# Optimization experiments

Measured on AMD Instinct MI355X. Metric: run time of the kernel, lower is better.

The kernel has to match this reference:

```python
import jax, jax.numpy as jnp
import numpy as np

DECAY = 0.99
EPS = 1e-5
COMMIT_W = 1.0


def setup_inputs() -> dict:
    key = jax.random.key(0)
    k1, k2, k3 = jax.random.split(key, 3)
    N, D, K = 65536, 64, 2048
    x = jax.random.normal(k1, (N, D), dtype=jnp.float32)
    embed = jax.random.normal(k2, (K, D), dtype=jnp.float32)
    embed_avg = jax.random.normal(k3, (K, D), dtype=jnp.float32)
    cluster_size = jnp.ones((K,), dtype=jnp.float32)
    return {"x": x, "embed": embed, "embed_avg": embed_avg, "cluster_size": cluster_size}


def reference(x, embed, embed_avg, cluster_size):
    # x: [N, D], embed: [K, D]
    K = embed.shape[0]
    # squared euclidean distances [N, K] (the cdist step)
    x2 = jnp.sum(x * x, axis=-1, keepdims=True)            # [N, 1]
    e2 = jnp.sum(embed * embed, axis=-1)                    # [K]
    dist = x2 - 2.0 * (x @ embed.T) + e2[None, :]           # [N, K]
    embed_ind = jnp.argmin(dist, axis=-1)                   # [N]

    # codebook gather + straight-through estimator
    quantize = embed[embed_ind]                              # [N, D]
    commit_loss = COMMIT_W * jnp.mean((jax.lax.stop_gradient(quantize) - x) ** 2)
    quantize_st = x + jax.lax.stop_gradient(quantize - x)

    # EMA codebook update (scatter / segment-sum, no gradient)
    ones = jnp.ones(embed_ind.shape, dtype=x.dtype)
    counts = jax.ops.segment_sum(ones, embed_ind, num_segments=K)        # [K]
    embed_sum = jax.ops.segment_sum(x, embed_ind, num_segments=K)        # [K, D]
    new_cluster_size = DECAY * cluster_size + (1.0 - DECAY) * counts
    new_embed_avg = DECAY * embed_avg + (1.0 - DECAY) * embed_sum
    n = jnp.sum(new_cluster_size)
    smoothed = (new_cluster_size + EPS) / (n + K * EPS) * n              # laplace smoothing
    new_embed = new_embed_avg / smoothed[:, None]                         # [K, D]

    return quantize_st, commit_loss, embed_ind, new_embed
```

## Files before the change

### kernel.cpp

```cpp
#include <hip/hip_runtime.h>
#include <hip/hip_bf16.h>

#define N_ROWS 65536
#define DIM 64
#define KC 2048
#define NPHH 16
#define DECAY_F 0.99f
#define OMD_F 0.01f
#define EPS_F 1e-5f
#define MARGIN 0.005f

typedef short  s16x8  __attribute__((ext_vector_type(8)));
typedef __bf16 bf16x8 __attribute__((ext_vector_type(8)));
typedef float  f32x4v __attribute__((ext_vector_type(4)));

__device__ __forceinline__ bf16x8 as_bf(s16x8 v) { return __builtin_bit_cast(bf16x8, v); }

static constexpr size_t WS_E2       = 0;
static constexpr size_t WS_SMOOTH   = 2048;
static constexpr size_t WS_OFFS     = 4096;
static constexpr size_t WS_ROWIDS   = 6144;
static constexpr size_t WS_EH       = 71680;
static constexpr size_t WS_EL       = 137216;
static constexpr size_t WS_COUNTS   = 202752;
static constexpr size_t WS_CURS     = 204800;
static constexpr size_t WS_LOSS     = 206848;
static constexpr size_t WS_FLAGCNT  = 206849;
static constexpr size_t WS_ESUM     = 206852;
static constexpr size_t WS_FLAGLIST = 337924;
static constexpr size_t WS_ZERO_CNT = 4098;

__device__ __forceinline__ unsigned short bf16_rne(float f) {
    unsigned u = __float_as_uint(f);
    return (unsigned short)((u + 0x7FFFu + ((u >> 16) & 1u)) >> 16);
}

__global__ __launch_bounds__(256) void vq_prep_e_kernel(
    const float* __restrict__ embed, float* __restrict__ ws) {
    const int tid = threadIdx.x;
    const int lane = tid & 63;
    const int k = blockIdx.x * 4 + (tid >> 6);

    const int gtid = blockIdx.x * 256 + tid;
    if (gtid < (int)WS_ZERO_CNT) ws[WS_COUNTS + gtid] = 0.f;
    ws[WS_ESUM + gtid] = 0.f;

    float v = embed[(size_t)k * DIM + lane];
    float m2v = -2.f * v;
    unsigned short hb = bf16_rne(m2v);
    float hf = __uint_as_float((unsigned)hb << 16);
    unsigned short lb = bf16_rne(m2v - hf);
    ((short*)(ws + WS_EH))[(size_t)k * DIM + lane] = (short)hb;
    ((short*)(ws + WS_EL))[(size_t)k * DIM + lane] = (short)lb;

    float sq = v * v;
#pragma unroll
    for (int off = 32; off > 0; off >>= 1)
        sq += __shfl_down(sq, off, 64);
    if (lane == 0) ws[WS_E2 + k] = sq;
}

__global__ __launch_bounds__(512, 4) void vq_mfma_kernel(
    const float* __restrict__ x,
    const float* __restrict__ embed,
    float* __restrict__ ws,
    float* __restrict__ out_q,
    float* __restrict__ out_ind) {
    __shared__ __attribute__((aligned(16))) short tile_lds[2][2][16][512];
    __shared__ __attribute__((aligned(16))) float e2_lds[KC];
    __shared__ float mb1[128], mb2[128];
    __shared__ int   mi1[128];

    const int tid = threadIdx.x;
    const int lane = tid & 63;
    const int w = tid >> 6;
    const int kh = w >> 2;
    const int wq = w & 3;
    const int row0 = blockIdx.x * 128 + wq * 32;
    const int cr = lane & 15;
    const int g = lane >> 4;

    {
        const float4* s4p = reinterpret_cast<const float4*>(ws + WS_E2);
        *reinterpret_cast<float4*>(&e2_lds[tid * 4]) = s4p[tid];
    }

    s16x8 xh[2][2], xl[2][2];
#pragma unroll
    for (int f = 0; f < 2; ++f) {
#pragma unroll
        for (int kc = 0; kc < 2; ++kc) {
            const float4* p4 = reinterpret_cast<const float4*>(
                x + (size_t)(row0 + f * 16 + cr) * DIM + kc * 32 + g * 8);
            float4 u = p4[0], v = p4[1];
            s16x8 h, l;
            unsigned short hb;
            hb = bf16_rne(u.x); h[0] = (short)hb; l[0] = (short)bf16_rne(u.x - __uint_as_float((unsigned)hb << 16));
            hb = bf16_rne(u.y); h[1] = (short)hb; l[1] = (short)bf16_rne(u.y - __uint_as_float((unsigned)hb << 16));
            hb = bf16_rne(u.z); h[2] = (short)hb; l[2] = (short)bf16_rne(u.z - __uint_as_float((unsigned)hb << 16));
            hb = bf16_rne(u.w); h[3] = (short)hb; l[3] = (short)bf16_rne(u.w - __uint_as_float((unsigned)hb << 16));
            hb = bf16_rne(v.x); h[4] = (short)hb; l[4] = (short)bf16_rne(v.x - __uint_as_float((unsigned)hb << 16));
            hb = bf16_rne(v.y); h[5] = (short)hb; l[5] = (short)bf16_rne(v.y - __uint_as_float((unsigned)hb << 16));
            hb = bf16_rne(v.z); h[6] = (short)hb; l[6] = (short)bf16_rne(v.z - __uint_as_float((unsigned)hb << 16));
            hb = bf16_rne(v.w); h[7] = (short)hb; l[7] = (short)bf16_rne(v.w - __uint_as_float((unsigned)hb << 16));
            xh[f][kc] = h; xl[f][kc] = l;
        }
    }

    const short* ehp = (const short*)(ws + WS_EH);
    const short* elp = (const short*)(ws + WS_EL);

    const short* mat_base = ((wq < 2) ? ehp : elp) + (wq & 1) * 32;

#define STAGE(buf, ph)                                                                  \
    {                                                                                   \
        _Pragma("unroll")                                                               \
        for (int s4 = 0; s4 < 4; ++s4) {                                                \
            const short* gsrc = mat_base +                                              \
                (size_t)(((kh * NPHH + (ph)) * 64) + s4 * 16 + cr) * DIM + g * 8;       \
            __builtin_amdgcn_global_load_lds(                                           \
                (const __attribute__((address_space(1))) void*)gsrc,                    \
                (__attribute__((address_space(3))) void*)(&tile_lds[(buf)][kh][s4 * 4 + wq][0]), \
                16, 0, 0);                                                              \
        }                                                                               \
    }

    STAGE(0, 0);
    __syncthreads();

    float b1[2] = {__builtin_inff(), __builtin_inff()};
    float b2[2] = {__builtin_inff(), __builtin_inff()};
    int   i1[2] = {0, 0};

    f32x4v accA[4][2], accB[4][2];

#define MFMA_PHASE(ph, WACC)                                                            \
    {                                                                                   \
        const int cur_ = (ph) & 1;                                                      \
        if ((ph) + 1 < NPHH) STAGE(cur_ ^ 1, (ph) + 1);                                 \
        __builtin_amdgcn_s_setprio(1);                                                  \
        _Pragma("unroll")                                                               \
        for (int s = 0; s < 4; ++s) {                                                   \
            s16x8 eh0 = *(const s16x8*)(&tile_lds[cur_][kh][s * 4 + 0][lane * 8]);      \
            s16x8 eh1 = *(const s16x8*)(&tile_lds[cur_][kh][s * 4 + 1][lane * 8]);      \
            s16x8 el0 = *(const s16x8*)(&tile_lds[cur_][kh][s * 4 + 2][lane * 8]);      \
            s16x8 el1 = *(const s16x8*)(&tile_lds[cur_][kh][s * 4 + 3][lane * 8]);      \
            const int kb_ = (kh * NPHH + (ph)) * 64 + s * 16 + g * 4;                   \
            f32x4v e2v = *reinterpret_cast<const f32x4v*>(&e2_lds[kb_]);                \
            _Pragma("unroll")                                                           \
            for (int f = 0; f < 2; ++f) {                                               \
                f32x4v a = e2v;                                                         \
                a = __builtin_amdgcn_mfma_f32_16x16x32_bf16(as_bf(eh0), as_bf(xh[f][0]), a, 0, 0, 0); \
                a = __builtin_amdgcn_mfma_f32_16x16x32_bf16(as_bf(eh1), as_bf(xh[f][1]), a, 0, 0, 0); \
                a = __builtin_amdgcn_mfma_f32_16x16x32_bf16(as_bf(el0), as_bf(xh[f][0]), a, 0, 0, 0); \
                a = __builtin_amdgcn_mfma_f32_16x16x32_bf16(as_bf(el1), as_bf(xh[f][1]), a, 0, 0, 0); \
                a = __builtin_amdgcn_mfma_f32_16x16x32_bf16(as_bf(eh0), as_bf(xl[f][0]), a, 0, 0, 0); \
                a = __builtin_amdgcn_mfma_f32_16x16x32_bf16(as_bf(eh1), as_bf(xl[f][1]), a, 0, 0, 0); \
                WACC[s][f] = a;                                                         \
            }                                                                           \
        }                                                                               \
        __builtin_amdgcn_s_setprio(0);                                                  \
    }

#define SELECT_PHASE(ph, RACC)                                                          \
    {                                                                                   \
        _Pragma("unroll")                                                               \
        for (int s = 0; s < 4; ++s) {                                                   \
            const int kb_ = (kh * NPHH + (ph)) * 64 + s * 16 + g * 4;                   \
            _Pragma("unroll")                                                           \
            for (int f = 0; f < 2; ++f) {                                               \
                _Pragma("unroll")                                                       \
                for (int r = 0; r < 4; ++r) {                                           \
                    float dd = RACC[s][f][r];                                           \
                    b2[f] = __builtin_amdgcn_fmed3f(b1[f], b2[f], dd);                  \
                    if (dd < b1[f]) { b1[f] = dd; i1[f] = kb_ + r; }                    \
                }                                                                       \
            }                                                                           \
        }                                                                               \
    }

    MFMA_PHASE(0, accA);
    __syncthreads();
    for (int ph = 1; ph < NPHH - 1; ph += 2) {
        MFMA_PHASE(ph, accB);
        SELECT_PHASE(ph - 1, accA);
        __syncthreads();
        MFMA_PHASE(ph + 1, accA);
        SELECT_PHASE(ph, accB);
        __syncthreads();
    }
    MFMA_PHASE(NPHH - 1, accB);
    SELECT_PHASE(NPHH - 2, accA);
    SELECT_PHASE(NPHH - 1, accB);
#undef MFMA_PHASE
#undef SELECT_PHASE
#undef STAGE

#pragma unroll
    for (int f = 0; f < 2; ++f) {
#pragma unroll
        for (int mask = 16; mask <= 32; mask <<= 1) {
            float ob1 = __shfl_xor(b1[f], mask, 64);
            int   oi1 = __shfl_xor(i1[f], mask, 64);
            float ob2 = __shfl_xor(b2[f], mask, 64);
            float nb2 = fminf(fminf(b2[f], ob2), fmaxf(b1[f], ob1));
            if (ob1 < b1[f] || (ob1 == b1[f] && oi1 < i1[f])) { b1[f] = ob1; i1[f] = oi1; }
            b2[f] = nb2;
        }
    }

    if (kh == 1 && g == 0) {
#pragma unroll
        for (int f = 0; f < 2; ++f) {
            int rib = wq * 32 + f * 16 + cr;
            mb1[rib] = b1[f];
            mb2[rib] = b2[f];
            mi1[rib] = i1[f];
        }
    }
    __syncthreads();
    if (kh == 1) return;

    float gap[2];
#pragma unroll
    for (int f = 0; f < 2; ++f) {
        int rib = wq * 32 + f * 16 + cr;
        float ob1 = mb1[rib];
        float ob2 = mb2[rib];
        int   oi1 = mi1[rib];
        float nb2 = fminf(fminf(b2[f], ob2), fmaxf(b1[f], ob1));
        if (ob1 < b1[f]) { b1[f] = ob1; i1[f] = oi1; }
        b2[f] = nb2;
        gap[f] = b2[f] - b1[f];
        if (g == 0) {
            int row = row0 + f * 16 + cr;
            out_ind[row] = (float)i1[f];
            if (gap[f] < MARGIN) {
                int p = atomicAdd((int*)(ws + WS_FLAGCNT), 1);
                if (p >= 0 && p < N_ROWS) ((int*)(ws + WS_FLAGLIST))[p] = row;
            } else {
                atomicAdd((int*)(ws + WS_COUNTS) + i1[f], 1);
            }
        }
    }

    float lossacc = 0.f;
#pragma unroll
    for (int f = 0; f < 2; ++f) {
#pragma unroll
        for (int r = 0; r < 16; ++r) {
            int   fi_r = __shfl(i1[f], r, 64);
            float gp_r = __shfl(gap[f], r, 64);
            if (gp_r >= MARGIN) {
                int row = row0 + f * 16 + r;
                float q  = embed[(size_t)fi_r * DIM + lane];
                float xv = x[(size_t)row * DIM + lane];
                out_q[(size_t)row * DIM + lane] = q;
                float d = q - xv;
                lossacc = fmaf(d, d, lossacc);
            }
        }
    }
#pragma unroll
    for (int off = 32; off > 0; off >>= 1)
        lossacc += __shfl_down(lossacc, off, 64);
    if (lane == 0) atomicAdd(ws + WS_LOSS, lossacc);
}

__global__ __launch_bounds__(256) void vq_rescore_kernel(
    const float* __restrict__ x,
    const float* __restrict__ embed,
    float* __restrict__ ws,
    float* __restrict__ out_q,
    float* __restrict__ out_ind) {
    __shared__ float xs[DIM];
    __shared__ float bd[256];
    __shared__ int   bi[256];
    __shared__ int   smi;
    const int tid = threadIdx.x;
    int cnt = ((const int*)(ws + WS_FLAGCNT))[0];
    cnt = (cnt < 0) ? 0 : ((cnt > N_ROWS) ? N_ROWS : cnt);
    const int* flags = (const int*)(ws + WS_FLAGLIST);

    for (int f = blockIdx.x; f < cnt; f += gridDim.x) {
        const int row = flags[f] & (N_ROWS - 1);
        if (tid < DIM) xs[tid] = x[(size_t)row * DIM + tid];
        __syncthreads();
        float lb = __builtin_inff(); int li = 0;
        for (int k = tid; k < KC; k += 256) {
            const float* e = embed + (size_t)k * DIM;
            float dot = 0.f;
#pragma unroll
            for (int d = 0; d < DIM; ++d) dot = fmaf(xs[d], e[d], dot);
            float dd = ws[WS_E2 + k] - 2.f * dot;
            if (dd < lb) { lb = dd; li = k; }
        }
        bd[tid] = lb; bi[tid] = li;
        __syncthreads();
        for (int s = 128; s > 0; s >>= 1) {
            if (tid < s) {
                float ov = bd[tid + s]; int oi = bi[tid + s];
                if (ov < bd[tid] || (ov == bd[tid] && oi < bi[tid])) { bd[tid] = ov; bi[tid] = oi; }
            }
            __syncthreads();
        }
        if (tid == 0) {
            out_ind[row] = (float)bi[0];
            smi = bi[0];
            atomicAdd((int*)(ws + WS_COUNTS) + bi[0], 1);
        }
        __syncthreads();
        const int mi = smi;
        if (tid < DIM) {
            float q = embed[(size_t)mi * DIM + tid];
            float xv = xs[tid];
            out_q[(size_t)row * DIM + tid] = q;
            float d = q - xv;
            float ld = d * d;
#pragma unroll
            for (int off = 32; off > 0; off >>= 1)
                ld += __shfl_down(ld, off, 64);
            if (tid == 0) atomicAdd(ws + WS_LOSS, ld);
        }
        __syncthreads();
    }
}

__global__ __launch_bounds__(256) void vq_prefix_kernel(
    const float* __restrict__ cluster_size,
    float* __restrict__ ws,
    float* __restrict__ out_loss) {
    __shared__ int   sscan[256];
    __shared__ float sred[256];
    const int tid = threadIdx.x;
    const int* counts = (const int*)(ws + WS_COUNTS);
    int* offs = (int*)(ws + WS_OFFS);

    int lc[8];
    int tot = 0;
    float csum = 0.f;
#pragma unroll
    for (int j = 0; j < 8; ++j) {
        lc[j] = counts[tid * 8 + j];
        tot += lc[j];
        csum += cluster_size[tid * 8 + j];
    }
    sscan[tid] = tot;
    sred[tid] = csum;
    __syncthreads();
    for (int off = 1; off < 256; off <<= 1) {
        int v = (tid >= off) ? sscan[tid - off] : 0;
        __syncthreads();
        sscan[tid] += v;
        __syncthreads();
    }
    for (int s = 128; s > 0; s >>= 1) {
        if (tid < s) sred[tid] += sred[tid + s];
        __syncthreads();
    }
    int run = sscan[tid] - tot;
#pragma unroll
    for (int j = 0; j < 8; ++j) {
        offs[tid * 8 + j] = run;
        run += lc[j];
    }
    const float n = DECAY_F * sred[0] + OMD_F * (float)N_ROWS;
    const float scale = n / (n + (float)KC * EPS_F);
#pragma unroll
    for (int j = 0; j < 8; ++j) {
        int k = tid * 8 + j;
        float ncs = fmaf(OMD_F, (float)counts[k], DECAY_F * cluster_size[k]);
        ws[WS_SMOOTH + k] = (ncs + EPS_F) * scale;
    }
    if (tid == 0) out_loss[0] = ws[WS_LOSS] / (float)((size_t)N_ROWS * DIM);
}

__global__ __launch_bounds__(256) void vq_fill_kernel(
    const float* __restrict__ out_ind,
    float* __restrict__ ws) {
    const int row = blockIdx.x * blockDim.x + threadIdx.x;
    const int fi = ((int)out_ind[row]) & (KC - 1);
    const int* offs = (const int*)(ws + WS_OFFS);
    int* curs = (int*)(ws + WS_CURS);
    int* rowids = (int*)(ws + WS_ROWIDS);
    int pos = atomicAdd(&curs[fi], 1);
    int idx = offs[fi] + pos;
    if (idx >= 0 && idx < N_ROWS) rowids[idx] = row | (fi << 16);
}

__global__ __launch_bounds__(256) void vq_gather_kernel(
    const float* __restrict__ x,
    float* __restrict__ ws) {
    const int lane = threadIdx.x & 63;
    const int w = blockIdx.x * 4 + (threadIdx.x >> 6);
    const int* rowids = (const int*)(ws + WS_ROWIDS);
    float* esum = ws + WS_ESUM;

    const int e = rowids[w * 32 + (lane & 31)];

    float pf[8];
#pragma unroll
    for (int j = 0; j < 8; ++j) {
        int rj = __shfl(e, j, 64) & 0xFFFF;
        pf[j] = x[(size_t)rj * DIM + lane];
    }

    float acc = 0.f;
    int kprev = (__shfl(e, 0, 64) >> 16) & (KC - 1);
#pragma unroll
    for (int i = 0; i < 32; ++i) {
        float v = pf[i & 7];
        if (i + 8 < 32) {
            int rn = __shfl(e, i + 8, 64) & 0xFFFF;
            pf[i & 7] = x[(size_t)rn * DIM + lane];
        }
        int k = (__shfl(e, i, 64) >> 16) & (KC - 1);
        if (k != kprev) {
            atomicAdd(&esum[(size_t)kprev * DIM + lane], acc);
            acc = 0.f;
            kprev = k;
        }
        acc += v;
    }
    atomicAdd(&esum[(size_t)kprev * DIM + lane], acc);
}

__global__ __launch_bounds__(256) void vq_emb_kernel(
    const float* __restrict__ embed_avg,
    const float* __restrict__ ws,
    float* __restrict__ out_embed) {
    int i = blockIdx.x * blockDim.x + threadIdx.x;
    if (i >= KC * DIM) return;
    int k = i >> 6;
    float na = fmaf(OMD_F, ws[WS_ESUM + i], DECAY_F * embed_avg[i]);
    out_embed[i] = na / ws[WS_SMOOTH + k];
}

extern "C" void kernel_launch(void* const* d_in, const int* in_sizes, int n_in,
                              void* d_out, int out_size, void* d_ws, size_t ws_size,
                              hipStream_t stream) {
    const float* x            = (const float*)d_in[0];
    const float* embed        = (const float*)d_in[1];
    const float* embed_avg    = (const float*)d_in[2];
    const float* cluster_size = (const float*)d_in[3];

    float* out      = (float*)d_out;
    float* out_q    = out;
    float* out_loss = out + (size_t)N_ROWS * DIM;
    float* out_ind  = out_loss + 1;
    float* out_emb  = out_ind + N_ROWS;

    float* ws = (float*)d_ws;

    vq_prep_e_kernel<<<KC / 4, 256, 0, stream>>>(embed, ws);
    vq_mfma_kernel<<<N_ROWS / 128, 512, 0, stream>>>(x, embed, ws, out_q, out_ind);
    vq_rescore_kernel<<<2048, 256, 0, stream>>>(x, embed, ws, out_q, out_ind);
    vq_prefix_kernel<<<1, 256, 0, stream>>>(cluster_size, ws, out_loss);
    vq_fill_kernel<<<N_ROWS / 256, 256, 0, stream>>>(out_ind, ws);
    vq_gather_kernel<<<N_ROWS / 32 / 4, 256, 0, stream>>>(x, ws);
    vq_emb_kernel<<<(KC * DIM) / 256, 256, 0, stream>>>(embed_avg, ws, out_emb);
}
```

Before: 144.0 us.

## Switch distance MFMA from 16x16x32 to 32x32x16 bf16 tiles

Replaces the 16x16x32 bf16 MFMA tiling of the split-bf16 distance GEMM with 32x32x16 instructions, so each wave handles a 32-row by 32-code block per instruction. The LDS tile layout, staging indices, x fragment layout and cross-lane argmin reduction are all reworked to match, and the e2 bias is now added during selection instead of seeding the accumulator. Part of the selection is also moved inside the MFMA phase for the first block. The goal is fewer MFMA issues and fewer redundant LDS reads per FLOP. In exchange, the larger 16-register accumulators raise register pressure and the MFMA chains are longer and serial.

```diff
diff --git a/kernel.cpp b/kernel.cpp
--- a/kernel.cpp
+++ b/kernel.cpp
@@ -13,6 +13,7 @@
 typedef short  s16x8  __attribute__((ext_vector_type(8)));
 typedef __bf16 bf16x8 __attribute__((ext_vector_type(8)));
 typedef float  f32x4v __attribute__((ext_vector_type(4)));
+typedef float  f32x16 __attribute__((ext_vector_type(16)));
 
 __device__ __forceinline__ bf16x8 as_bf(s16x8 v) { return __builtin_bit_cast(bf16x8, v); }
 
@@ -66,7 +67,7 @@
     float* __restrict__ ws,
     float* __restrict__ out_q,
     float* __restrict__ out_ind) {
-    __shared__ __attribute__((aligned(16))) short tile_lds[2][2][16][512];
+    __shared__ __attribute__((aligned(16))) short tile_lds[2][2][2][8][512];
     __shared__ __attribute__((aligned(16))) float e2_lds[KC];
     __shared__ float mb1[128], mb2[128];
     __shared__ int   mi1[128];
@@ -77,50 +78,49 @@
     const int kh = w >> 2;
     const int wq = w & 3;
     const int row0 = blockIdx.x * 128 + wq * 32;
-    const int cr = lane & 15;
-    const int g = lane >> 4;
+    const int c32 = lane & 31;
+    const int h = lane >> 5;
 
     {
         const float4* s4p = reinterpret_cast<const float4*>(ws + WS_E2);
         *reinterpret_cast<float4*>(&e2_lds[tid * 4]) = s4p[tid];
     }
 
-    s16x8 xh[2][2], xl[2][2];
-#pragma unroll
-    for (int f = 0; f < 2; ++f) {
-#pragma unroll
-        for (int kc = 0; kc < 2; ++kc) {
-            const float4* p4 = reinterpret_cast<const float4*>(
-                x + (size_t)(row0 + f * 16 + cr) * DIM + kc * 32 + g * 8);
-            float4 u = p4[0], v = p4[1];
-            s16x8 h, l;
-            unsigned short hb;
-            hb = bf16_rne(u.x); h[0] = (short)hb; l[0] = (short)bf16_rne(u.x - __uint_as_float((unsigned)hb << 16));
-            hb = bf16_rne(u.y); h[1] = (short)hb; l[1] = (short)bf16_rne(u.y - __uint_as_float((unsigned)hb << 16));
-            hb = bf16_rne(u.z); h[2] = (short)hb; l[2] = (short)bf16_rne(u.z - __uint_as_float((unsigned)hb << 16));
-            hb = bf16_rne(u.w); h[3] = (short)hb; l[3] = (short)bf16_rne(u.w - __uint_as_float((unsigned)hb << 16));
-            hb = bf16_rne(v.x); h[4] = (short)hb; l[4] = (short)bf16_rne(v.x - __uint_as_float((unsigned)hb << 16));
-            hb = bf16_rne(v.y); h[5] = (short)hb; l[5] = (short)bf16_rne(v.y - __uint_as_float((unsigned)hb << 16));
-            hb = bf16_rne(v.z); h[6] = (short)hb; l[6] = (short)bf16_rne(v.z - __uint_as_float((unsigned)hb << 16));
-            hb = bf16_rne(v.w); h[7] = (short)hb; l[7] = (short)bf16_rne(v.w - __uint_as_float((unsigned)hb << 16));
-            xh[f][kc] = h; xl[f][kc] = l;
-        }
+    s16x8 xh[4], xl[4];
+#pragma unroll
+    for (int c = 0; c < 4; ++c) {
+        const float4* p4 = reinterpret_cast<const float4*>(
+            x + (size_t)(row0 + c32) * DIM + c * 16 + h * 8);
+        float4 u = p4[0], v = p4[1];
+        s16x8 hh, ll;
+        unsigned short hb;
+        hb = bf16_rne(u.x); hh[0] = (short)hb; ll[0] = (short)bf16_rne(u.x - __uint_as_float((unsigned)hb << 16));
+        hb = bf16_rne(u.y); hh[1] = (short)hb; ll[1] = (short)bf16_rne(u.y - __uint_as_float((unsigned)hb << 16));
+        hb = bf16_rne(u.z); hh[2] = (short)hb; ll[2] = (short)bf16_rne(u.z - __uint_as_float((unsigned)hb << 16));
+        hb = bf16_rne(u.w); hh[3] = (short)hb; ll[3] = (short)bf16_rne(u.w - __uint_as_float((unsigned)hb << 16));
+        hb = bf16_rne(v.x); hh[4] = (short)hb; ll[4] = (short)bf16_rne(v.x - __uint_as_float((unsigned)hb << 16));
+        hb = bf16_rne(v.y); hh[5] = (short)hb; ll[5] = (short)bf16_rne(v.y - __uint_as_float((unsigned)hb << 16));
+        hb = bf16_rne(v.z); hh[6] = (short)hb; ll[6] = (short)bf16_rne(v.z - __uint_as_float((unsigned)hb << 16));
+        hb = bf16_rne(v.w); hh[7] = (short)hb; ll[7] = (short)bf16_rne(v.w - __uint_as_float((unsigned)hb << 16));
+        xh[c] = hh; xl[c] = ll;
     }
 
     const short* ehp = (const short*)(ws + WS_EH);
     const short* elp = (const short*)(ws + WS_EL);
 
-    const short* mat_base = ((wq < 2) ? ehp : elp) + (wq & 1) * 32;
-
 #define STAGE(buf, ph)                                                                  \
     {                                                                                   \
         _Pragma("unroll")                                                               \
-        for (int s4 = 0; s4 < 4; ++s4) {                                                \
-            const short* gsrc = mat_base +                                              \
-                (size_t)(((kh * NPHH + (ph)) * 64) + s4 * 16 + cr) * DIM + g * 8;       \
+        for (int j = 0; j < 4; ++j) {                                                   \
+            const int fm = wq * 4 + j;                                                  \
+            const int blk = fm >> 3, m = fm & 7;                                        \
+            const int term = m >> 2, chunk = m & 3;                                     \
+            const int code0 = ((kh * NPHH + (ph)) * 64) + blk * 32;                     \
+            const short* gsrc = (term ? elp : ehp) +                                    \
+                (size_t)(code0 + c32) * DIM + chunk * 16 + h * 8;                       \
             __builtin_amdgcn_global_load_lds(                                           \
                 (const __attribute__((address_space(1))) void*)gsrc,                    \
-                (__attribute__((address_space(3))) void*)(&tile_lds[(buf)][kh][s4 * 4 + wq][0]), \
+                (__attribute__((address_space(3))) void*)(&tile_lds[(buf)][kh][blk][m][0]), \
                 16, 0, 0);                                                              \
         }                                                                               \
     }
@@ -128,55 +128,73 @@
     STAGE(0, 0);
     __syncthreads();
 
-    float b1[2] = {__builtin_inff(), __builtin_inff()};
-    float b2[2] = {__builtin_inff(), __builtin_inff()};
-    int   i1[2] = {0, 0};
-
-    f32x4v accA[4][2], accB[4][2];
+    float b1 = __builtin_inff(), b2 = __builtin_inff();
+    int   i1 = 0;
+
+    f32x16 accA, accB;
+
+#define SEL1(dd_, kidx_)                                                                \
+    {                                                                                   \
+        b2 = __builtin_amdgcn_fmed3f(b1, b2, (dd_));                                    \
+        if ((dd_) < b1) { b1 = (dd_); i1 = (kidx_); }                                   \
+    }
+
+#define SELECT_BLK(code0_, AV)                                                          \
+    {                                                                                   \
+        _Pragma("unroll")                                                               \
+        for (int q = 0; q < 4; ++q) {                                                   \
+            f32x4v e2v = *reinterpret_cast<const f32x4v*>(&e2_lds[(code0_) + q * 8 + h * 4]); \
+            _Pragma("unroll")                                                           \
+            for (int jj = 0; jj < 4; ++jj) {                                            \
+                float dd = AV[q * 4 + jj] + e2v[jj];                                    \
+                SEL1(dd, (code0_) + q * 8 + h * 4 + jj);                                \
+            }                                                                           \
+        }                                                                               \
+    }
+
+#define MFMA_BLK(cur_, blk_, AV)                                                        \
+    {                                                                                   \
+        s16x8 e0 = *(const s16x8*)(&tile_lds[cur_][kh][blk_][0][lane * 8]);             \
+        s16x8 e1 = *(const s16x8*)(&tile_lds[cur_][kh][blk_][1][lane * 8]);             \
+        s16x8 e2f = *(const s16x8*)(&tile_lds[cur_][kh][blk_][2][lane * 8]);            \
+        s16x8 e3 = *(const s16x8*)(&tile_lds[cur_][kh][blk_][3][lane * 8]);             \
+        s16x8 l0 = *(const s16x8*)(&tile_lds[cur_][kh][blk_][4][lane * 8]);             \
+        s16x8 l1 = *(const s16x8*)(&tile_lds[cur_][kh][blk_][5][lane * 8]);             \
+        s16x8 l2 = *(const s16x8*)(&tile_lds[cur_][kh][blk_][6][lane * 8]);             \
+        s16x8 l3 = *(const s16x8*)(&tile_lds[cur_][kh][blk_][7][lane * 8]);             \
+        f32x16 a = {};                                                                  \
+        a = __builtin_amdgcn_mfma_f32_32x32x16_bf16(as_bf(e0), as_bf(xh[0]), a, 0, 0, 0); \
+        a = __builtin_amdgcn_mfma_f32_32x32x16_bf16(as_bf(e1), as_bf(xh[1]), a, 0, 0, 0); \
+        a = __builtin_amdgcn_mfma_f32_32x32x16_bf16(as_bf(e2f), as_bf(xh[2]), a, 0, 0, 0); \
+        a = __builtin_amdgcn_mfma_f32_32x32x16_bf16(as_bf(e3), as_bf(xh[3]), a, 0, 0, 0); \
+        a = __builtin_amdgcn_mfma_f32_32x32x16_bf16(as_bf(l0), as_bf(xh[0]), a, 0, 0, 0); \
+        a = __builtin_amdgcn_mfma_f32_32x32x16_bf16(as_bf(l1), as_bf(xh[1]), a, 0, 0, 0); \
+        a = __builtin_amdgcn_mfma_f32_32x32x16_bf16(as_bf(l2), as_bf(xh[2]), a, 0, 0, 0); \
+        a = __builtin_amdgcn_mfma_f32_32x32x16_bf16(as_bf(l3), as_bf(xh[3]), a, 0, 0, 0); \
+        a = __builtin_amdgcn_mfma_f32_32x32x16_bf16(as_bf(e0), as_bf(xl[0]), a, 0, 0, 0); \
+        a = __builtin_amdgcn_mfma_f32_32x32x16_bf16(as_bf(e1), as_bf(xl[1]), a, 0, 0, 0); \
+        a = __builtin_amdgcn_mfma_f32_32x32x16_bf16(as_bf(e2f), as_bf(xl[2]), a, 0, 0, 0); \
+        a = __builtin_amdgcn_mfma_f32_32x32x16_bf16(as_bf(e3), as_bf(xl[3]), a, 0, 0, 0); \
+        AV = a;                                                                         \
+    }
 
 #define MFMA_PHASE(ph, WACC)                                                            \
     {                                                                                   \
         const int cur_ = (ph) & 1;                                                      \
         if ((ph) + 1 < NPHH) STAGE(cur_ ^ 1, (ph) + 1);                                 \
         __builtin_amdgcn_s_setprio(1);                                                  \
-        _Pragma("unroll")                                                               \
-        for (int s = 0; s < 4; ++s) {                                                   \
-            s16x8 eh0 = *(const s16x8*)(&tile_lds[cur_][kh][s * 4 + 0][lane * 8]);      \
-            s16x8 eh1 = *(const s16x8*)(&tile_lds[cur_][kh][s * 4 + 1][lane * 8]);      \
-            s16x8 el0 = *(const s16x8*)(&tile_lds[cur_][kh][s * 4 + 2][lane * 8]);      \
-            s16x8 el1 = *(const s16x8*)(&tile_lds[cur_][kh][s * 4 + 3][lane * 8]);      \
-            const int kb_ = (kh * NPHH + (ph)) * 64 + s * 16 + g * 4;                   \
-            f32x4v e2v = *reinterpret_cast<const f32x4v*>(&e2_lds[kb_]);                \
-            _Pragma("unroll")                                                           \
-            for (int f = 0; f < 2; ++f) {                                               \
-                f32x4v a = e2v;                                                         \
-                a = __builtin_amdgcn_mfma_f32_16x16x32_bf16(as_bf(eh0), as_bf(xh[f][0]), a, 0, 0, 0); \
-                a = __builtin_amdgcn_mfma_f32_16x16x32_bf16(as_bf(eh1), as_bf(xh[f][1]), a, 0, 0, 0); \
-                a = __builtin_amdgcn_mfma_f32_16x16x32_bf16(as_bf(el0), as_bf(xh[f][0]), a, 0, 0, 0); \
-                a = __builtin_amdgcn_mfma_f32_16x16x32_bf16(as_bf(el1), as_bf(xh[f][1]), a, 0, 0, 0); \
-                a = __builtin_amdgcn_mfma_f32_16x16x32_bf16(as_bf(eh0), as_bf(xl[f][0]), a, 0, 0, 0); \
-                a = __builtin_amdgcn_mfma_f32_16x16x32_bf16(as_bf(eh1), as_bf(xl[f][1]), a, 0, 0, 0); \
-                WACC[s][f] = a;                                                         \
-            }                                                                           \
-        }                                                                               \
+        const int cbase_ = ((kh * NPHH + (ph)) * 64);                                   \
+        f32x16 a0_;                                                                     \
+        MFMA_BLK(cur_, 0, a0_);                                                         \
+        MFMA_BLK(cur_, 1, WACC);                                                        \
+        SELECT_BLK(cbase_, a0_);                                                        \
         __builtin_amdgcn_s_setprio(0);                                                  \
     }
 
 #define SELECT_PHASE(ph, RACC)                                                          \
     {                                                                                   \
-        _Pragma("unroll")                                                               \
-        for (int s = 0; s < 4; ++s) {                                                   \
-            const int kb_ = (kh * NPHH + (ph)) * 64 + s * 16 + g * 4;                   \
-            _Pragma("unroll")                                                           \
-            for (int f = 0; f < 2; ++f) {                                               \
-                _Pragma("unroll")                                                       \
-                for (int r = 0; r < 4; ++r) {                                           \
-                    float dd = RACC[s][f][r];                                           \
-                    b2[f] = __builtin_amdgcn_fmed3f(b1[f], b2[f], dd);                  \
-                    if (dd < b1[f]) { b1[f] = dd; i1[f] = kb_ + r; }                    \
-                }                                                                       \
-            }                                                                           \
-        }                                                                               \
+        const int cbase_ = ((kh * NPHH + (ph)) * 64) + 32;                              \
+        SELECT_BLK(cbase_, RACC);                                                       \
     }
 
     MFMA_PHASE(0, accA);
@@ -194,71 +212,63 @@
     SELECT_PHASE(NPHH - 1, accB);
 #undef MFMA_PHASE
 #undef SELECT_PHASE
+#undef MFMA_BLK
+#undef SELECT_BLK
+#undef SEL1
 #undef STAGE
 
-#pragma unroll
-    for (int f = 0; f < 2; ++f) {
-#pragma unroll
-        for (int mask = 16; mask <= 32; mask <<= 1) {
-            float ob1 = __shfl_xor(b1[f], mask, 64);
-            int   oi1 = __shfl_xor(i1[f], mask, 64);
-            float ob2 = __shfl_xor(b2[f], mask, 64);
-            float nb2 = fminf(fminf(b2[f], ob2), fmaxf(b1[f], ob1));
-            if (ob1 < b1[f] || (ob1 == b1[f] && oi1 < i1[f])) { b1[f] = ob1; i1[f] = oi1; }
-            b2[f] = nb2;
-        }
-    }
-
-    if (kh == 1 && g == 0) {
-#pragma unroll
-        for (int f = 0; f < 2; ++f) {
-            int rib = wq * 32 + f * 16 + cr;
-            mb1[rib] = b1[f];
-            mb2[rib] = b2[f];
-            mi1[rib] = i1[f];
-        }
+    {
+        float ob1 = __shfl_xor(b1, 32, 64);
+        int   oi1 = __shfl_xor(i1, 32, 64);
+        float ob2 = __shfl_xor(b2, 32, 64);
+        float nb2 = fminf(fminf(b2, ob2), fmaxf(b1, ob1));
+        if (ob1 < b1 || (ob1 == b1 && oi1 < i1)) { b1 = ob1; i1 = oi1; }
+        b2 = nb2;
+    }
+
+    if (kh == 1 && h == 0) {
+        int rib = wq * 32 + c32;
+        mb1[rib] = b1;
+        mb2[rib] = b2;
+        mi1[rib] = i1;
     }
     __syncthreads();
     if (kh == 1) return;
 
-    float gap[2];
-#pragma unroll
-    for (int f = 0; f < 2; ++f) {
-        int rib = wq * 32 + f * 16 + cr;
+    float gap;
+    {
+        int rib = wq * 32 + c32;
         float ob1 = mb1[rib];
         float ob2 = mb2[rib];
         int   oi1 = mi1[rib];
-        float nb2 = fminf(fminf(b2[f], ob2), fmaxf(b1[f], ob1));
-        if (ob1 < b1[f]) { b1[f] = ob1; i1[f] = oi1; }
-        b2[f] = nb2;
-        gap[f] = b2[f] - b1[f];
-        if (g == 0) {
-            int row = row0 + f * 16 + cr;
-            out_ind[row] = (float)i1[f];
-            if (gap[f] < MARGIN) {
+        float nb2 = fminf(fminf(b2, ob2), fmaxf(b1, ob1));
+        if (ob1 < b1) { b1 = ob1; i1 = oi1; }
+        b2 = nb2;
+        gap = b2 - b1;
+        if (h == 0) {
+            int row = row0 + c32;
+            out_ind[row] = (float)i1;
+            if (gap < MARGIN) {
                 int p = atomicAdd((int*)(ws + WS_FLAGCNT), 1);
                 if (p >= 0 && p < N_ROWS) ((int*)(ws + WS_FLAGLIST))[p] = row;
             } else {
-                atomicAdd((int*)(ws + WS_COUNTS) + i1[f], 1);
+                atomicAdd((int*)(ws + WS_COUNTS) + i1, 1);
             }
         }
     }
 
     float lossacc = 0.f;
 #pragma unroll
-    for (int f = 0; f < 2; ++f) {
-#pragma unroll
-        for (int r = 0; r < 16; ++r) {
-            int   fi_r = __shfl(i1[f], r, 64);
-            float gp_r = __shfl(gap[f], r, 64);
-            if (gp_r >= MARGIN) {
-                int row = row0 + f * 16 + r;
-                float q  = embed[(size_t)fi_r * DIM + lane];
-                float xv = x[(size_t)row * DIM + lane];
-                out_q[(size_t)row * DIM + lane] = q;
-                float d = q - xv;
-                lossacc = fmaf(d, d, lossacc);
-            }
+    for (int r = 0; r < 32; ++r) {
+        int   fi_r = __shfl(i1, r, 64);
+        float gp_r = __shfl(gap, r, 64);
+        if (gp_r >= MARGIN) {
+            int row = row0 + r;
+            float q  = embed[(size_t)fi_r * DIM + lane];
+            float xv = x[(size_t)row * DIM + lane];
+            out_q[(size_t)row * DIM + lane] = q;
+            float d = q - xv;
+            lossacc = fmaf(d, d, lossacc);
         }
     }
 #pragma unroll
```

After: 147.9 us. 1.03x slower.
